# Performance work log

Hardware: AMD Instinct MI355X
Metric: run time of the kernel (lower is better)

Reference implementation:

```python
import jax, jax.numpy as jnp
import numpy as np

T, N = 12, 1000          # frames, pedestrians
RNN, EMB, GS, OUT = 128, 64, 4, 5
G = GS * GS              # 16 grid cells


def lstm_cell(x, h, c, W_ih, W_hh, b_ih, b_hh):
    # PyTorch LSTMCell gate order: i, f, g, o
    gates = x @ W_ih.T + h @ W_hh.T + b_ih + b_hh
    i, f, g, o = jnp.split(gates, 4, axis=-1)
    c_new = jax.nn.sigmoid(f) * c + jax.nn.sigmoid(i) * jnp.tanh(g)
    h_new = jax.nn.sigmoid(o) * jnp.tanh(c_new)
    return h_new, c_new


def setup_inputs() -> dict:
    key = jax.random.key(0)
    ks = jax.random.split(key, 10)
    s = 0.02  # small init scale for weights
    # binary occupancy grid masks: grid[f, n, p, g] = 1 if ped p falls in cell g of ped n's neighborhood
    grids = (jax.random.uniform(ks[1], (T, N, N, G)) < 0.02).astype(jnp.float32)
    return {
        "input_data": jax.random.normal(ks[0], (T, N, 2), dtype=jnp.float32),
        "grids": grids,
        "hidden_states": jnp.zeros((N, RNN), dtype=jnp.float32),
        "cell_states": jnp.zeros((N, RNN), dtype=jnp.float32),
        "W_in": jax.random.normal(ks[2], (EMB, 2)) * s,
        "b_in": jnp.zeros((EMB,), dtype=jnp.float32),
        "W_soc": jax.random.normal(ks[3], (EMB, G * RNN)) * s,
        "b_soc": jnp.zeros((EMB,), dtype=jnp.float32),
        "W_ih": jax.random.normal(ks[4], (4 * RNN, 2 * EMB)) * s,
        "W_hh": jax.random.normal(ks[5], (4 * RNN, RNN)) * s,
        "b_ih": jnp.zeros((4 * RNN,), dtype=jnp.float32),
        "b_hh": jnp.zeros((4 * RNN,), dtype=jnp.float32),
        "W_out": jax.random.normal(ks[6], (OUT, RNN)) * s,
        "b_out": jnp.zeros((OUT,), dtype=jnp.float32),
    }


def reference(input_data, grids, hidden_states, cell_states,
              W_in, b_in, W_soc, b_soc, W_ih, W_hh, b_ih, b_hh, W_out, b_out):
    def step(carry, frame):
        h, c = carry
        x, grid = frame  # x: [N,2], grid: [N,N,G]
        # social pooling: for each node n, grid[n].T @ h  -> [G, RNN]
        social = jnp.einsum('npg,ph->ngh', grid, h).reshape(N, G * RNN)
        ie = jax.nn.relu(x @ W_in.T + b_in)           # [N, EMB]
        te = jax.nn.relu(social @ W_soc.T + b_soc)    # [N, EMB]
        emb = jnp.concatenate([ie, te], axis=-1)      # [N, 2*EMB]
        h, c = lstm_cell(emb, h, c, W_ih, W_hh, b_ih, b_hh)
        out = h @ W_out.T + b_out                     # [N, OUT]
        return (h, c), out

    (h, c), outputs = jax.lax.scan(step, (hidden_states, cell_states),
                                   (input_data, grids))
    return outputs, h, c  # outputs: [T, N, OUT]
```

## Files before the change

kernel.cpp:

```cpp
#include <hip/hip_runtime.h>


#define TT    12
#define NN    1000
#define RNNW  128
#define OUTD  5
#define GROW  16000
#define UCW   1024
#define NCHK  63

__device__ __forceinline__ float sigmf(float x) { return 1.f / (1.f + __expf(-x)); }

__global__ void k_prep(const float* __restrict__ h0, const float* __restrict__ c0,
                       const float* __restrict__ W_soc,
                       const float* __restrict__ W_ih, const float* __restrict__ W_hh,
                       const float* __restrict__ b_ih, const float* __restrict__ b_hh,
                       float* __restrict__ h, float* __restrict__ c,
                       float* __restrict__ WsT, float* __restrict__ WcT,
                       float* __restrict__ bsum) {
    int i = blockIdx.x * 256 + threadIdx.x;
    if (i < 131072) {
        int e = i >> 11, gk = i & 2047;
        WsT[gk * 64 + e] = W_soc[i];
    } else if (i < 196608) {
        int i2 = i - 131072;
        int j = i2 >> 7, k = i2 & 127;
        int j2 = (j & 127) * 4 + (j >> 7);
        WcT[k * 512 + j2] = W_ih[i2];
    } else if (i < 262144) {
        int i3 = i - 196608;
        int j = i3 >> 7, k = i3 & 127;
        int j2 = (j & 127) * 4 + (j >> 7);
        WcT[(128 + k) * 512 + j2] = W_hh[i3];
    } else if (i < 262656) {
        int j = i - 262144;
        int j2 = (j & 127) * 4 + (j >> 7);
        bsum[j2] = b_ih[j] + b_hh[j];
    } else if (i < 262656 + NN * RNNW) {
        int i4 = i - 262656; h[i4] = h0[i4];
    } else if (i < 262656 + 2 * NN * RNNW) {
        int i5 = i - 262656 - NN * RNNW; c[i5] = c0[i5];
    }
}

__global__ __launch_bounds__(256) void k_U(const float* __restrict__ h,
                                           const float* __restrict__ WsT,
                                           const float* __restrict__ W_out,
                                           const float* __restrict__ b_out,
                                           float* __restrict__ U,
                                           float* __restrict__ out, int t) {
    __shared__ float sAT[RNNW][64];
    __shared__ float sBT[RNNW][64];
    const int tid = threadIdx.x;
    const int p0 = blockIdx.x * 64;
    const int g  = blockIdx.y;
    {
        int pp = tid >> 2, kq = (tid & 3) * 4;
        int p = p0 + pp;
        #pragma unroll
        for (int pass = 0; pass < 8; ++pass) {
            int k0 = pass * 16 + kq;
            float4 v = {0.f, 0.f, 0.f, 0.f};
            if (p < NN) v = *(const float4*)(h + (size_t)p * RNNW + k0);
            sAT[k0 + 0][pp] = v.x; sAT[k0 + 1][pp] = v.y;
            sAT[k0 + 2][pp] = v.z; sAT[k0 + 3][pp] = v.w;
        }
    }
    {
        #pragma unroll
        for (int pass = 0; pass < 8; ++pass) {
            int f = pass * 256 + tid;
            int k = f >> 4, e4 = (f & 15) * 4;
            float4 v = *(const float4*)(WsT + (size_t)(g * 128 + k) * 64 + e4);
            *(float4*)(&sBT[k][e4]) = v;
        }
    }
    __syncthreads();
    const int tx = tid & 15, ty = tid >> 4;
    float acc[4][4];
    #pragma unroll
    for (int i = 0; i < 4; i++)
        #pragma unroll
        for (int j = 0; j < 4; j++) acc[i][j] = 0.f;
    #pragma unroll 4
    for (int k = 0; k < RNNW; ++k) {
        float4 a4 = *(const float4*)(&sAT[k][ty * 4]);
        float4 b4 = *(const float4*)(&sBT[k][tx * 4]);
        const float av[4] = {a4.x, a4.y, a4.z, a4.w};
        const float bv[4] = {b4.x, b4.y, b4.z, b4.w};
        #pragma unroll
        for (int i = 0; i < 4; i++)
            #pragma unroll
            for (int j = 0; j < 4; j++) acc[i][j] += av[i] * bv[j];
    }
    #pragma unroll
    for (int i = 0; i < 4; i++) {
        int p = p0 + ty * 4 + i;
        if (p < NN) {
            float4 v = {acc[i][0], acc[i][1], acc[i][2], acc[i][3]};
            *(float4*)(U + (size_t)p * UCW + g * 64 + tx * 4) = v;
        }
    }
    if (t >= 0 && g == 0) {
        for (int task = tid; task < 64 * OUTD; task += 256) {
            int pp = task / OUTD, d = task - pp * OUTD;
            int p = p0 + pp;
            if (p < NN) {
                float s = b_out[d];
                const float* wr = W_out + d * RNNW;
                for (int k = 0; k < RNNW; ++k) s += sAT[k][pp] * wr[k];
                out[((size_t)t * NN + p) * OUTD + d] = s;
            }
        }
    }
}

__global__ __launch_bounds__(512) void k_pool(const unsigned int* __restrict__ grd,
                                              const float* __restrict__ x_in,
                                              const float* __restrict__ U,
                                              const float* __restrict__ W_in,
                                              const float* __restrict__ b_in,
                                              const float* __restrict__ b_soc,
                                              float* __restrict__ A, int t) {
    const int n = blockIdx.x;
    const int tid = threadIdx.x;
    const int lane = tid & 63, wv = tid >> 6;
    const unsigned int* gp = grd + ((size_t)t * NN + n) * (size_t)GROW;
    float ac0 = 0.f, ac1 = 0.f, ac2 = 0.f, ac3 = 0.f;
    for (int it = 0; it < 8; ++it) {
        int cc = it * 8 + wv;
        if (cc >= NCHK) break;
        int f0 = cc * 256 + lane * 4;
        uint4 v = {0u, 0u, 0u, 0u};
        if (f0 < GROW) v = *(const uint4*)(gp + f0);
        unsigned long long m0 = __ballot(v.x != 0u);
        unsigned long long m1 = __ballot(v.y != 0u);
        unsigned long long m2 = __ballot(v.z != 0u);
        unsigned long long m3 = __ballot(v.w != 0u);
        const int base = cc * 256;
        while (m0 | m1 | m2 | m3) {
            float u0 = 0.f, u1 = 0.f, u2 = 0.f, u3 = 0.f;
            if (m0) { int b = __builtin_ctzll(m0); m0 &= m0 - 1;
                      int f = base + b * 4 + 0;
                      u0 = U[(size_t)(f >> 4) * UCW + (f & 15) * 64 + lane]; }
            if (m1) { int b = __builtin_ctzll(m1); m1 &= m1 - 1;
                      int f = base + b * 4 + 1;
                      u1 = U[(size_t)(f >> 4) * UCW + (f & 15) * 64 + lane]; }
            if (m2) { int b = __builtin_ctzll(m2); m2 &= m2 - 1;
                      int f = base + b * 4 + 2;
                      u2 = U[(size_t)(f >> 4) * UCW + (f & 15) * 64 + lane]; }
            if (m3) { int b = __builtin_ctzll(m3); m3 &= m3 - 1;
                      int f = base + b * 4 + 3;
                      u3 = U[(size_t)(f >> 4) * UCW + (f & 15) * 64 + lane]; }
            ac0 += u0; ac1 += u1; ac2 += u2; ac3 += u3;
        }
    }
    __shared__ float sAcc[8][64];
    sAcc[wv][lane] = (ac0 + ac1) + (ac2 + ac3);
    __syncthreads();
    if (tid < 64) {
        float s = 0.f;
        #pragma unroll
        for (int w = 0; w < 8; w++) s += sAcc[w][tid];
        float te = fmaxf(s + b_soc[tid], 0.f);
        float x0 = x_in[((size_t)t * NN + n) * 2 + 0];
        float x1 = x_in[((size_t)t * NN + n) * 2 + 1];
        float ie = fmaxf(W_in[tid * 2 + 0] * x0 + W_in[tid * 2 + 1] * x1 + b_in[tid], 0.f);
        A[(size_t)n * RNNW + tid]      = ie;
        A[(size_t)n * RNNW + 64 + tid] = te;
    }
}

__global__ __launch_bounds__(256) void k_gl(const float* __restrict__ A,
                                            const float* __restrict__ hin,
                                            float* __restrict__ hout,
                                            float* __restrict__ c,
                                            const float* __restrict__ WcT,
                                            const float* __restrict__ bsum,
                                            float* __restrict__ out, int t) {
    __shared__ float sAT[128][32];
    __shared__ float sBT[128][64];
    const int tid = threadIdx.x;
    const int n0 = blockIdx.x * 32;
    const int j0 = blockIdx.y * 64;
    const int tx = tid & 15, ty = tid >> 4;
    float acc[2][4];
    #pragma unroll
    for (int i = 0; i < 2; i++)
        #pragma unroll
        for (int j = 0; j < 4; j++) acc[i][j] = 0.f;
    for (int kc = 0; kc < 2; ++kc) {
        __syncthreads();
        {
            int nn = tid >> 3, kq = (tid & 7) * 4;
            int n = n0 + nn;
            const float* src = kc ? (hin + (size_t)n * RNNW) : (A + (size_t)n * RNNW);
            #pragma unroll
            for (int pass = 0; pass < 4; ++pass) {
                int k0 = pass * 32 + kq;
                float4 v = {0.f, 0.f, 0.f, 0.f};
                if (n < NN) v = *(const float4*)(src + k0);
                sAT[k0 + 0][nn] = v.x; sAT[k0 + 1][nn] = v.y;
                sAT[k0 + 2][nn] = v.z; sAT[k0 + 3][nn] = v.w;
            }
        }
        {
            #pragma unroll
            for (int pass = 0; pass < 8; ++pass) {
                int f = pass * 256 + tid;
                int k = f >> 4, e4 = (f & 15) * 4;
                float4 v = *(const float4*)(WcT + (size_t)(kc * 128 + k) * 512 + j0 + e4);
                *(float4*)(&sBT[k][e4]) = v;
            }
        }
        __syncthreads();
        #pragma unroll 4
        for (int k = 0; k < 128; ++k) {
            float2 a2 = *(const float2*)(&sAT[k][ty * 2]);
            float4 b4 = *(const float4*)(&sBT[k][tx * 4]);
            const float av[2] = {a2.x, a2.y};
            const float bv[4] = {b4.x, b4.y, b4.z, b4.w};
            #pragma unroll
            for (int i = 0; i < 2; i++)
                #pragma unroll
                for (int j = 0; j < 4; j++) acc[i][j] += av[i] * bv[j];
        }
    }
    float4 bs = *(const float4*)(bsum + j0 + tx * 4);
    const int r = (j0 >> 2) + tx;
    #pragma unroll
    for (int i = 0; i < 2; i++) {
        int n = n0 + ty * 2 + i;
        if (n < NN) {
            float gi = acc[i][0] + bs.x;
            float gf = acc[i][1] + bs.y;
            float gg = acc[i][2] + bs.z;
            float go = acc[i][3] + bs.w;
            float cn = sigmf(gf) * c[(size_t)n * RNNW + r] + sigmf(gi) * tanhf(gg);
            float hn = sigmf(go) * tanhf(cn);
            c[(size_t)n * RNNW + r] = cn;
            hout[(size_t)n * RNNW + r] = hn;
            if (t == TT - 1) {
                out[(size_t)TT * NN * OUTD + (size_t)n * RNNW + r] = hn;
                out[(size_t)TT * NN * OUTD + (size_t)NN * RNNW + (size_t)n * RNNW + r] = cn;
            }
        }
    }
}

__global__ __launch_bounds__(256) void k_tail(const float* __restrict__ h,
                                              const float* __restrict__ W_out,
                                              const float* __restrict__ b_out,
                                              float* __restrict__ out) {
    int task = blockIdx.x * 256 + threadIdx.x;
    if (task < NN * OUTD) {
        int p = task / OUTD, d = task - p * OUTD;
        float s = b_out[d];
        const float* wr = W_out + d * RNNW;
        const float* hp = h + (size_t)p * RNNW;
        for (int k = 0; k < RNNW; ++k) s += hp[k] * wr[k];
        out[((size_t)(TT - 1) * NN + p) * OUTD + d] = s;
    }
}

extern "C" void kernel_launch(void* const* d_in, const int* in_sizes, int n_in,
                              void* d_out, int out_size, void* d_ws, size_t ws_size,
                              hipStream_t stream) {
    const float* x_in       = (const float*)d_in[0];
    const unsigned int* grd = (const unsigned int*)d_in[1];
    const float* h0         = (const float*)d_in[2];
    const float* c0         = (const float*)d_in[3];
    const float* W_in       = (const float*)d_in[4];
    const float* b_in       = (const float*)d_in[5];
    const float* W_soc      = (const float*)d_in[6];
    const float* b_soc      = (const float*)d_in[7];
    const float* W_ih       = (const float*)d_in[8];
    const float* W_hh       = (const float*)d_in[9];
    const float* b_ih       = (const float*)d_in[10];
    const float* b_hh       = (const float*)d_in[11];
    const float* W_out      = (const float*)d_in[12];
    const float* b_out      = (const float*)d_in[13];
    float* out = (float*)d_out;

    float* hb0  = (float*)d_ws;
    float* hb1  = hb0 + NN * RNNW;
    float* c    = hb1 + NN * RNNW;
    float* U    = c + NN * RNNW;
    float* A    = U + (size_t)NN * UCW;
    float* WsT  = A + (size_t)NN * RNNW;
    float* WcT  = WsT + 131072;
    float* bsum = WcT + 131072;

    hipLaunchKernelGGL(k_prep, dim3(2026), dim3(256), 0, stream,
                       h0, c0, W_soc, W_ih, W_hh, b_ih, b_hh, hb0, c, WsT, WcT, bsum);
    hipLaunchKernelGGL(k_U, dim3(16, 16), dim3(256), 0, stream,
                       hb0, WsT, W_out, b_out, U, out, -1);
    for (int t = 0; t < TT; ++t) {
        float* hin  = (t & 1) ? hb1 : hb0;
        float* hout = (t & 1) ? hb0 : hb1;
        hipLaunchKernelGGL(k_pool, dim3(NN), dim3(512), 0, stream,
                           grd, x_in, U, W_in, b_in, b_soc, A, t);
        hipLaunchKernelGGL(k_gl, dim3(32, 8), dim3(256), 0, stream,
                           A, hin, hout, c, WcT, bsum, out, t);
        if (t < TT - 1) {
            hipLaunchKernelGGL(k_U, dim3(16, 16), dim3(256), 0, stream,
                               hout, WsT, W_out, b_out, U, out, t);
        }
    }
    hipLaunchKernelGGL(k_tail, dim3(20), dim3(256), 0, stream,
                       hb0, W_out, b_out, out);
}
```

Before: 641.8 us.

## Compact nonzero grid indices into shared memory before gathering in social pooling

The pooling kernel now runs in two phases. It first scans the grid row with 16 wavefronts, using ballot and popcount to compact nonzero flat indices into per-wave shared-memory lists. It then spreads the gathers of U rows across all waves, processing two indices per iteration. This removes the divergent per-wave ballot loops with uneven work and exposes more independent loads. In exchange it uses 32KB of shared memory and 1024-thread blocks, which may reduce occupancy, and adds a block barrier.

```diff
diff --git a/kernel.cpp b/kernel.cpp
--- a/kernel.cpp
+++ b/kernel.cpp
@@ -115,53 +115,70 @@
     }
 }
 
-__global__ __launch_bounds__(512) void k_pool(const unsigned int* __restrict__ grd,
-                                              const float* __restrict__ x_in,
-                                              const float* __restrict__ U,
-                                              const float* __restrict__ W_in,
-                                              const float* __restrict__ b_in,
-                                              const float* __restrict__ b_soc,
-                                              float* __restrict__ A, int t) {
+__global__ __launch_bounds__(1024) void k_pool(const unsigned int* __restrict__ grd,
+                                               const float* __restrict__ x_in,
+                                               const float* __restrict__ U,
+                                               const float* __restrict__ W_in,
+                                               const float* __restrict__ b_in,
+                                               const float* __restrict__ b_soc,
+                                               float* __restrict__ A, int t) {
+    __shared__ unsigned short sIdx[16 * 1024];
+    __shared__ int sCnt[16];
+    __shared__ float sAcc[16][64];
     const int n = blockIdx.x;
     const int tid = threadIdx.x;
     const int lane = tid & 63, wv = tid >> 6;
     const unsigned int* gp = grd + ((size_t)t * NN + n) * (size_t)GROW;
-    float ac0 = 0.f, ac1 = 0.f, ac2 = 0.f, ac3 = 0.f;
-    for (int it = 0; it < 8; ++it) {
-        int cc = it * 8 + wv;
-        if (cc >= NCHK) break;
-        int f0 = cc * 256 + lane * 4;
-        uint4 v = {0u, 0u, 0u, 0u};
-        if (f0 < GROW) v = *(const uint4*)(gp + f0);
-        unsigned long long m0 = __ballot(v.x != 0u);
-        unsigned long long m1 = __ballot(v.y != 0u);
-        unsigned long long m2 = __ballot(v.z != 0u);
-        unsigned long long m3 = __ballot(v.w != 0u);
-        const int base = cc * 256;
-        while (m0 | m1 | m2 | m3) {
-            float u0 = 0.f, u1 = 0.f, u2 = 0.f, u3 = 0.f;
-            if (m0) { int b = __builtin_ctzll(m0); m0 &= m0 - 1;
-                      int f = base + b * 4 + 0;
-                      u0 = U[(size_t)(f >> 4) * UCW + (f & 15) * 64 + lane]; }
-            if (m1) { int b = __builtin_ctzll(m1); m1 &= m1 - 1;
-                      int f = base + b * 4 + 1;
-                      u1 = U[(size_t)(f >> 4) * UCW + (f & 15) * 64 + lane]; }
-            if (m2) { int b = __builtin_ctzll(m2); m2 &= m2 - 1;
-                      int f = base + b * 4 + 2;
-                      u2 = U[(size_t)(f >> 4) * UCW + (f & 15) * 64 + lane]; }
-            if (m3) { int b = __builtin_ctzll(m3); m3 &= m3 - 1;
-                      int f = base + b * 4 + 3;
-                      u3 = U[(size_t)(f >> 4) * UCW + (f & 15) * 64 + lane]; }
-            ac0 += u0; ac1 += u1; ac2 += u2; ac3 += u3;
-        }
-    }
-    __shared__ float sAcc[8][64];
-    sAcc[wv][lane] = (ac0 + ac1) + (ac2 + ac3);
+    const unsigned long long lmask = (1ull << lane) - 1ull;
+
+    {
+        int wcnt = 0;
+        unsigned short* seg = sIdx + wv * 1024;
+        #pragma unroll
+        for (int it = 0; it < 4; ++it) {
+            int c = it * 16 + wv;
+            if (c >= NCHK) break;
+            int f0 = c * 256 + lane * 4;
+            uint4 v = {0u, 0u, 0u, 0u};
+            if (f0 < GROW) v = *(const uint4*)(gp + f0);
+            unsigned int va[4] = {v.x, v.y, v.z, v.w};
+            #pragma unroll
+            for (int sub = 0; sub < 4; ++sub) {
+                bool nz = (va[sub] != 0u);
+                unsigned long long m = __ballot(nz);
+                if (nz) {
+                    int pos = wcnt + __popcll(m & lmask);
+                    seg[pos] = (unsigned short)(f0 + sub);
+                }
+                wcnt += __popcll(m);
+            }
+        }
+        if (lane == 0) sCnt[wv] = wcnt;
+    }
+    __syncthreads();
+    {
+        float a0 = 0.f, a1 = 0.f;
+        for (int s = 0; s < 16; ++s) {
+            const int cnt = sCnt[s];
+            const unsigned short* seg = sIdx + s * 1024;
+            int i = wv;
+            for (; i + 16 < cnt; i += 32) {
+                int f0 = seg[i], f1 = seg[i + 16];
+                a0 += U[(size_t)(f0 >> 4) * UCW + (f0 & 15) * 64 + lane];
+                a1 += U[(size_t)(f1 >> 4) * UCW + (f1 & 15) * 64 + lane];
+            }
+            if (i < cnt) {
+                int f = seg[i];
+                a0 += U[(size_t)(f >> 4) * UCW + (f & 15) * 64 + lane];
+            }
+        }
+        sAcc[wv][lane] = a0 + a1;
+    }
     __syncthreads();
     if (tid < 64) {
         float s = 0.f;
         #pragma unroll
-        for (int w = 0; w < 8; w++) s += sAcc[w][tid];
+        for (int w = 0; w < 16; w++) s += sAcc[w][tid];
         float te = fmaxf(s + b_soc[tid], 0.f);
         float x0 = x_in[((size_t)t * NN + n) * 2 + 0];
         float x1 = x_in[((size_t)t * NN + n) * 2 + 1];
@@ -298,7 +315,7 @@
     for (int t = 0; t < TT; ++t) {
         float* hin  = (t & 1) ? hb1 : hb0;
         float* hout = (t & 1) ? hb0 : hb1;
-        hipLaunchKernelGGL(k_pool, dim3(NN), dim3(512), 0, stream,
+        hipLaunchKernelGGL(k_pool, dim3(NN), dim3(1024), 0, stream,
                            grd, x_in, U, W_in, b_in, b_soc, A, t);
         hipLaunchKernelGGL(k_gl, dim3(32, 8), dim3(256), 0, stream,
                            A, hin, hout, c, WcT, bsum, out, t);
```

Measured after the change: 668.9 us. 1.04x slower.

## Fuse LSTM gate kernel with social projection via atomic-counter inter-block handoff

Applied to the files above, without the earlier changes.

Merges the LSTM gate/cell kernel and the per-step U projection (plus output head) into one launch, where the last 256 blocks spin on a per-step atomic counter until all gate blocks have written h. The per-step output head and final tail kernel are folded into the consumer blocks. This removes one kernel launch per step and the tail launch. In exchange it relies on all producer blocks being scheduled before consumers spin, which risks deadlock or lost occupancy if consumer blocks are resident first.

```diff
diff --git a/kernel.cpp b/kernel.cpp
--- a/kernel.cpp
+++ b/kernel.cpp
@@ -17,7 +17,7 @@
                        const float* __restrict__ b_ih, const float* __restrict__ b_hh,
                        float* __restrict__ h, float* __restrict__ c,
                        float* __restrict__ WsT, float* __restrict__ WcT,
-                       float* __restrict__ bsum) {
+                       float* __restrict__ bsum, unsigned int* __restrict__ ctr) {
     int i = blockIdx.x * 256 + threadIdx.x;
     if (i < 131072) {
         int e = i >> 11, gk = i & 2047;
@@ -36,19 +36,18 @@
         int j = i - 262144;
         int j2 = (j & 127) * 4 + (j >> 7);
         bsum[j2] = b_ih[j] + b_hh[j];
-    } else if (i < 262656 + NN * RNNW) {
+    } else if (i < 390656) {
         int i4 = i - 262656; h[i4] = h0[i4];
-    } else if (i < 262656 + 2 * NN * RNNW) {
-        int i5 = i - 262656 - NN * RNNW; c[i5] = c0[i5];
+    } else if (i < 518656) {
+        int i5 = i - 390656; c[i5] = c0[i5];
+    } else if (i < 518656 + TT) {
+        ctr[i - 518656] = 0u;
     }
 }
 
 __global__ __launch_bounds__(256) void k_U(const float* __restrict__ h,
                                            const float* __restrict__ WsT,
-                                           const float* __restrict__ W_out,
-                                           const float* __restrict__ b_out,
-                                           float* __restrict__ U,
-                                           float* __restrict__ out, int t) {
+                                           float* __restrict__ U) {
     __shared__ float sAT[RNNW][64];
     __shared__ float sBT[RNNW][64];
     const int tid = threadIdx.x;
@@ -99,18 +98,6 @@
         if (p < NN) {
             float4 v = {acc[i][0], acc[i][1], acc[i][2], acc[i][3]};
             *(float4*)(U + (size_t)p * UCW + g * 64 + tx * 4) = v;
-        }
-    }
-    if (t >= 0 && g == 0) {
-        for (int task = tid; task < 64 * OUTD; task += 256) {
-            int pp = task / OUTD, d = task - pp * OUTD;
-            int p = p0 + pp;
-            if (p < NN) {
-                float s = b_out[d];
-                const float* wr = W_out + d * RNNW;
-                for (int k = 0; k < RNNW; ++k) s += sAT[k][pp] * wr[k];
-                out[((size_t)t * NN + p) * OUTD + d] = s;
-            }
         }
     }
 }
@@ -171,95 +158,166 @@
     }
 }
 
-__global__ __launch_bounds__(256) void k_gl(const float* __restrict__ A,
-                                            const float* __restrict__ hin,
-                                            float* __restrict__ hout,
-                                            float* __restrict__ c,
-                                            const float* __restrict__ WcT,
-                                            const float* __restrict__ bsum,
-                                            float* __restrict__ out, int t) {
-    __shared__ float sAT[128][32];
-    __shared__ float sBT[128][64];
+__global__ __launch_bounds__(256) void k_glU(const float* __restrict__ A,
+                                             const float* __restrict__ hin,
+                                             float* __restrict__ hout,
+                                             float* __restrict__ c,
+                                             const float* __restrict__ WcT,
+                                             const float* __restrict__ bsum,
+                                             const float* __restrict__ WsT,
+                                             const float* __restrict__ W_out,
+                                             const float* __restrict__ b_out,
+                                             float* __restrict__ U,
+                                             float* __restrict__ out,
+                                             unsigned int* __restrict__ ctr, int t) {
+    __shared__ float smem[16384];
     const int tid = threadIdx.x;
-    const int n0 = blockIdx.x * 32;
-    const int j0 = blockIdx.y * 64;
-    const int tx = tid & 15, ty = tid >> 4;
-    float acc[2][4];
-    #pragma unroll
-    for (int i = 0; i < 2; i++)
-        #pragma unroll
-        for (int j = 0; j < 4; j++) acc[i][j] = 0.f;
-    for (int kc = 0; kc < 2; ++kc) {
+    const int bid = blockIdx.x;
+    if (bid < 256) {
+        float* sAT = smem;
+        float* sBT = smem + 4096;
+        const int n0 = (bid & 31) * 32;
+        const int j0 = (bid >> 5) * 64;
+        const int tx = tid & 15, ty = tid >> 4;
+        float acc[2][4];
+        #pragma unroll
+        for (int i = 0; i < 2; i++)
+            #pragma unroll
+            for (int j = 0; j < 4; j++) acc[i][j] = 0.f;
+        for (int kc = 0; kc < 2; ++kc) {
+            __syncthreads();
+            {
+                int nn = tid >> 3, kq = (tid & 7) * 4;
+                int n = n0 + nn;
+                const float* src = kc ? (hin + (size_t)n * RNNW) : (A + (size_t)n * RNNW);
+                #pragma unroll
+                for (int pass = 0; pass < 4; ++pass) {
+                    int k0 = pass * 32 + kq;
+                    float4 v = {0.f, 0.f, 0.f, 0.f};
+                    if (n < NN) v = *(const float4*)(src + k0);
+                    sAT[(k0 + 0) * 32 + nn] = v.x; sAT[(k0 + 1) * 32 + nn] = v.y;
+                    sAT[(k0 + 2) * 32 + nn] = v.z; sAT[(k0 + 3) * 32 + nn] = v.w;
+                }
+            }
+            {
+                #pragma unroll
+                for (int pass = 0; pass < 8; ++pass) {
+                    int f = pass * 256 + tid;
+                    int k = f >> 4, e4 = (f & 15) * 4;
+                    float4 v = *(const float4*)(WcT + (size_t)(kc * 128 + k) * 512 + j0 + e4);
+                    *(float4*)(&sBT[k * 64 + e4]) = v;
+                }
+            }
+            __syncthreads();
+            #pragma unroll 4
+            for (int k = 0; k < 128; ++k) {
+                float2 a2 = *(const float2*)(&sAT[k * 32 + ty * 2]);
+                float4 b4 = *(const float4*)(&sBT[k * 64 + tx * 4]);
+                const float av[2] = {a2.x, a2.y};
+                const float bv[4] = {b4.x, b4.y, b4.z, b4.w};
+                #pragma unroll
+                for (int i = 0; i < 2; i++)
+                    #pragma unroll
+                    for (int j = 0; j < 4; j++) acc[i][j] += av[i] * bv[j];
+            }
+        }
+        float4 bs = *(const float4*)(bsum + j0 + tx * 4);
+        const int r = (j0 >> 2) + tx;
+        #pragma unroll
+        for (int i = 0; i < 2; i++) {
+            int n = n0 + ty * 2 + i;
+            if (n < NN) {
+                float gi = acc[i][0] + bs.x;
+                float gf = acc[i][1] + bs.y;
+                float gg = acc[i][2] + bs.z;
+                float go = acc[i][3] + bs.w;
+                float cn = sigmf(gf) * c[(size_t)n * RNNW + r] + sigmf(gi) * tanhf(gg);
+                float hn = sigmf(go) * tanhf(cn);
+                c[(size_t)n * RNNW + r] = cn;
+                hout[(size_t)n * RNNW + r] = hn;
+                if (t == TT - 1) {
+                    out[(size_t)TT * NN * OUTD + (size_t)n * RNNW + r] = hn;
+                    out[(size_t)TT * NN * OUTD + (size_t)NN * RNNW + (size_t)n * RNNW + r] = cn;
+                }
+            }
+        }
+        __threadfence();
         __syncthreads();
+        if (tid == 0) atomicAdd(ctr + t, 1u);
+    } else {
+        const int ub = bid - 256;
+        const int p0 = (ub & 15) * 64;
+        const int g  = ub >> 4;
+        if (t == TT - 1 && g != 0) return;
+        if (tid == 0) {
+            while (__hip_atomic_load(ctr + t, __ATOMIC_ACQUIRE,
+                                     __HIP_MEMORY_SCOPE_AGENT) < 256u)
+                __builtin_amdgcn_s_sleep(8);
+        }
+        __syncthreads();
+        float* sAT = smem;
+        float* sBT = smem + 8192;
         {
-            int nn = tid >> 3, kq = (tid & 7) * 4;
-            int n = n0 + nn;
-            const float* src = kc ? (hin + (size_t)n * RNNW) : (A + (size_t)n * RNNW);
-            #pragma unroll
-            for (int pass = 0; pass < 4; ++pass) {
-                int k0 = pass * 32 + kq;
+            int pp = tid >> 2, kq = (tid & 3) * 4;
+            int p = p0 + pp;
+            #pragma unroll
+            for (int pass = 0; pass < 8; ++pass) {
+                int k0 = pass * 16 + kq;
                 float4 v = {0.f, 0.f, 0.f, 0.f};
-                if (n < NN) v = *(const float4*)(src + k0);
-                sAT[k0 + 0][nn] = v.x; sAT[k0 + 1][nn] = v.y;
-                sAT[k0 + 2][nn] = v.z; sAT[k0 + 3][nn] = v.w;
-            }
-        }
-        {
+                if (p < NN) v = *(const float4*)(hout + (size_t)p * RNNW + k0);
+                sAT[(k0 + 0) * 64 + pp] = v.x; sAT[(k0 + 1) * 64 + pp] = v.y;
+                sAT[(k0 + 2) * 64 + pp] = v.z; sAT[(k0 + 3) * 64 + pp] = v.w;
+            }
+        }
+        if (t < TT - 1) {
             #pragma unroll
             for (int pass = 0; pass < 8; ++pass) {
                 int f = pass * 256 + tid;
                 int k = f >> 4, e4 = (f & 15) * 4;
-                float4 v = *(const float4*)(WcT + (size_t)(kc * 128 + k) * 512 + j0 + e4);
-                *(float4*)(&sBT[k][e4]) = v;
+                float4 v = *(const float4*)(WsT + (size_t)(g * 128 + k) * 64 + e4);
+                *(float4*)(&sBT[k * 64 + e4]) = v;
             }
         }
         __syncthreads();
-        #pragma unroll 4
-        for (int k = 0; k < 128; ++k) {
-            float2 a2 = *(const float2*)(&sAT[k][ty * 2]);
-            float4 b4 = *(const float4*)(&sBT[k][tx * 4]);
-            const float av[2] = {a2.x, a2.y};
-            const float bv[4] = {b4.x, b4.y, b4.z, b4.w};
-            #pragma unroll
-            for (int i = 0; i < 2; i++)
-                #pragma unroll
-                for (int j = 0; j < 4; j++) acc[i][j] += av[i] * bv[j];
-        }
-    }
-    float4 bs = *(const float4*)(bsum + j0 + tx * 4);
-    const int r = (j0 >> 2) + tx;
-    #pragma unroll
-    for (int i = 0; i < 2; i++) {
-        int n = n0 + ty * 2 + i;
-        if (n < NN) {
-            float gi = acc[i][0] + bs.x;
-            float gf = acc[i][1] + bs.y;
-            float gg = acc[i][2] + bs.z;
-            float go = acc[i][3] + bs.w;
-            float cn = sigmf(gf) * c[(size_t)n * RNNW + r] + sigmf(gi) * tanhf(gg);
-            float hn = sigmf(go) * tanhf(cn);
-            c[(size_t)n * RNNW + r] = cn;
-            hout[(size_t)n * RNNW + r] = hn;
-            if (t == TT - 1) {
-                out[(size_t)TT * NN * OUTD + (size_t)n * RNNW + r] = hn;
-                out[(size_t)TT * NN * OUTD + (size_t)NN * RNNW + (size_t)n * RNNW + r] = cn;
-            }
-        }
-    }
-}
-
-__global__ __launch_bounds__(256) void k_tail(const float* __restrict__ h,
-                                              const float* __restrict__ W_out,
-                                              const float* __restrict__ b_out,
-                                              float* __restrict__ out) {
-    int task = blockIdx.x * 256 + threadIdx.x;
-    if (task < NN * OUTD) {
-        int p = task / OUTD, d = task - p * OUTD;
-        float s = b_out[d];
-        const float* wr = W_out + d * RNNW;
-        const float* hp = h + (size_t)p * RNNW;
-        for (int k = 0; k < RNNW; ++k) s += hp[k] * wr[k];
-        out[((size_t)(TT - 1) * NN + p) * OUTD + d] = s;
+        if (t < TT - 1) {
+            const int tx = tid & 15, ty = tid >> 4;
+            float acc[4][4];
+            #pragma unroll
+            for (int i = 0; i < 4; i++)
+                #pragma unroll
+                for (int j = 0; j < 4; j++) acc[i][j] = 0.f;
+            #pragma unroll 4
+            for (int k = 0; k < RNNW; ++k) {
+                float4 a4 = *(const float4*)(&sAT[k * 64 + ty * 4]);
+                float4 b4 = *(const float4*)(&sBT[k * 64 + tx * 4]);
+                const float av[4] = {a4.x, a4.y, a4.z, a4.w};
+                const float bv[4] = {b4.x, b4.y, b4.z, b4.w};
+                #pragma unroll
+                for (int i = 0; i < 4; i++)
+                    #pragma unroll
+                    for (int j = 0; j < 4; j++) acc[i][j] += av[i] * bv[j];
+            }
+            #pragma unroll
+            for (int i = 0; i < 4; i++) {
+                int p = p0 + ty * 4 + i;
+                if (p < NN) {
+                    float4 v = {acc[i][0], acc[i][1], acc[i][2], acc[i][3]};
+                    *(float4*)(U + (size_t)p * UCW + g * 64 + tx * 4) = v;
+                }
+            }
+        }
+        if (g == 0) {
+            for (int task = tid; task < 64 * OUTD; task += 256) {
+                int pp = task / OUTD, d = task - pp * OUTD;
+                int p = p0 + pp;
+                if (p < NN) {
+                    float s = b_out[d];
+                    const float* wr = W_out + d * RNNW;
+                    for (int k = 0; k < RNNW; ++k) s += sAT[k * 64 + pp] * wr[k];
+                    out[((size_t)t * NN + p) * OUTD + d] = s;
+                }
+            }
+        }
     }
 }
 
@@ -290,23 +348,19 @@
     float* WsT  = A + (size_t)NN * RNNW;
     float* WcT  = WsT + 131072;
     float* bsum = WcT + 131072;
-
-    hipLaunchKernelGGL(k_prep, dim3(2026), dim3(256), 0, stream,
-                       h0, c0, W_soc, W_ih, W_hh, b_ih, b_hh, hb0, c, WsT, WcT, bsum);
-    hipLaunchKernelGGL(k_U, dim3(16, 16), dim3(256), 0, stream,
-                       hb0, WsT, W_out, b_out, U, out, -1);
+    unsigned int* ctr = (unsigned int*)(bsum + 512);
+
+    hipLaunchKernelGGL(k_prep, dim3(2027), dim3(256), 0, stream,
+                       h0, c0, W_soc, W_ih, W_hh, b_ih, b_hh, hb0, c,
+                       WsT, WcT, bsum, ctr);
+    hipLaunchKernelGGL(k_U, dim3(16, 16), dim3(256), 0, stream, hb0, WsT, U);
     for (int t = 0; t < TT; ++t) {
         float* hin  = (t & 1) ? hb1 : hb0;
         float* hout = (t & 1) ? hb0 : hb1;
         hipLaunchKernelGGL(k_pool, dim3(NN), dim3(512), 0, stream,
                            grd, x_in, U, W_in, b_in, b_soc, A, t);
-        hipLaunchKernelGGL(k_gl, dim3(32, 8), dim3(256), 0, stream,
-                           A, hin, hout, c, WcT, bsum, out, t);
-        if (t < TT - 1) {
-            hipLaunchKernelGGL(k_U, dim3(16, 16), dim3(256), 0, stream,
-                               hout, WsT, W_out, b_out, U, out, t);
-        }
-    }
-    hipLaunchKernelGGL(k_tail, dim3(20), dim3(256), 0, stream,
-                       hb0, W_out, b_out, out);
-}
+        hipLaunchKernelGGL(k_glU, dim3(512), dim3(256), 0, stream,
+                           A, hin, hout, c, WcT, bsum, WsT, W_out, b_out,
+                           U, out, ctr, t);
+    }
+}
```

New measurement: 1.237 ms. +92.7%, slower.
